# Performance work log

Hardware: AMD Instinct MI355X
Metric: run time of the kernel (lower is better)

The kernel has to match this reference:

```python
import jax, jax.numpy as jnp
import numpy as np

S = 2048       # num tokens (one sequence)
H = 2048       # hidden size
D = 64         # head dim
HQ_SWA, HQ_HSA = 24, 8
HK_SWA, HK_HSA = 6, 2
WINDOW = 512   # sliding window size
THETA = 1e6
EPS = 1e-6
SCALE = D ** -0.5
NEG = -1e9


def setup_inputs() -> dict:
    key = jax.random.key(0)
    ks = jax.random.split(key, 9)
    def w(k, fan_in, fan_out):
        return jax.random.normal(k, (fan_in, fan_out), jnp.float32) * (1.0 / np.sqrt(fan_in))
    return {
        "hidden_states": jax.random.normal(ks[0], (S, H), jnp.float32),
        "positions": jnp.arange(S, dtype=jnp.int32),
        "wq_swa": w(ks[1], H, HQ_SWA * D),
        "wk_swa": w(ks[2], H, HK_SWA * D),
        "wv_swa": w(ks[3], H, HK_SWA * D),
        "wq_hsa": w(ks[4], H, HQ_HSA * D),
        "wk_hsa": w(ks[5], H, HK_HSA * D),
        "wv_hsa": w(ks[6], H, HK_HSA * D),
        "q_norm_w": jnp.ones((D,), jnp.float32),
        "k_norm_w": jnp.ones((D,), jnp.float32),
        "wo": w(ks[7], (HQ_SWA + HQ_HSA) * D, H),
    }


def _rmsnorm(x, w):
    # per-head RMSNorm over last dim (head_dim)
    var = jnp.mean(x * x, axis=-1, keepdims=True)
    return x * jax.lax.rsqrt(var + EPS) * w


def _rope(x, positions):
    # neox-style RoPE on [S, h, D]
    half = D // 2
    inv_freq = 1.0 / (THETA ** (jnp.arange(half, dtype=jnp.float32) / half))
    ang = positions.astype(jnp.float32)[:, None] * inv_freq  # [S, half]
    cos = jnp.cos(ang)[:, None, :]
    sin = jnp.sin(ang)[:, None, :]
    x1, x2 = x[..., :half], x[..., half:]
    return jnp.concatenate([x1 * cos - x2 * sin, x2 * cos + x1 * sin], axis=-1)


def _gqa_attn(q, k, v, mask):
    # q: [S, hq, D], k/v: [S, hk, D], mask: [S, S] bool (True = attend)
    hk = k.shape[1]
    g = q.shape[1] // hk
    qh = q.reshape(S, hk, g, D)
    scores = jnp.einsum('qhgd,khd->hgqk', qh, k) * SCALE
    scores = jnp.where(mask[None, None], scores, NEG)
    p = jax.nn.softmax(scores, axis=-1)
    out = jnp.einsum('hgqk,khd->qhgd', p, v)
    return out.reshape(S, hk * g * D)


def reference(hidden_states, positions, wq_swa, wk_swa, wv_swa,
              wq_hsa, wk_hsa, wv_hsa, q_norm_w, k_norm_w, wo):
    x = hidden_states
    # projections -> per-head layout
    swa_q = (x @ wq_swa).reshape(S, HQ_SWA, D)
    swa_k = (x @ wk_swa).reshape(S, HK_SWA, D)
    swa_v = (x @ wv_swa).reshape(S, HK_SWA, D)
    hsa_q = (x @ wq_hsa).reshape(S, HQ_HSA, D)
    hsa_k = (x @ wk_hsa).reshape(S, HK_HSA, D)
    hsa_v = (x @ wv_hsa).reshape(S, HK_HSA, D)
    # per-head RMSNorm on q and k (layerwise_qk_norm = False)
    swa_q = _rmsnorm(swa_q, q_norm_w)
    swa_k = _rmsnorm(swa_k, k_norm_w)
    hsa_q = _rmsnorm(hsa_q, q_norm_w)
    hsa_k = _rmsnorm(hsa_k, k_norm_w)
    # RoPE on SWA branch only (apply_hsa_rope = False)
    swa_q = _rope(swa_q, positions)
    swa_k = _rope(swa_k, positions)
    # masks
    i = jnp.arange(S)[:, None]
    j = jnp.arange(S)[None, :]
    causal = j <= i
    swa_mask = causal & ((i - j) < WINDOW)
    # SWA branch: sliding-window causal attention
    swa_out = _gqa_attn(swa_q, swa_k, swa_v, swa_mask)   # [S, HQ_SWA*D]
    # HSA branch: full-causal GQA attention (reference: all blocks retrieved)
    hsa_out = _gqa_attn(hsa_q, hsa_k, hsa_v, causal)     # [S, HQ_HSA*D]
    attn_out = jnp.concatenate([swa_out, hsa_out], axis=-1)
    return attn_out @ wo
```

## Files before the change

kernel.cpp:

```cpp
#include <hip/hip_runtime.h>

#define S_LEN 2048
#define QKV_N 3072

typedef __bf16 bf16_t;
typedef bf16_t b16x8 __attribute__((ext_vector_type(8)));
typedef unsigned short u16x8 __attribute__((ext_vector_type(8)));
typedef float f32x4 __attribute__((ext_vector_type(4)));
typedef unsigned int u32;
typedef __attribute__((address_space(3))) u32 lds_u32;
typedef __attribute__((address_space(1))) const u32 g_u32;

__device__ __forceinline__ void gload16(void* l, const void* g){
  __builtin_amdgcn_global_load_lds((g_u32*)g, (lds_u32*)l, 16, 0, 0);
}

__device__ __forceinline__ unsigned short f2b(float f){
  u32 u = __builtin_bit_cast(u32, f);
  u += 0x7fffu + ((u >> 16) & 1u);
  return (unsigned short)(u >> 16);
}

__global__ __launch_bounds__(256) void k_cvt(const float* __restrict__ x,
                                             unsigned short* __restrict__ y){
  int i = (blockIdx.x * 256 + threadIdx.x) * 4;
  float4 v = *reinterpret_cast<const float4*>(x + i);
  ushort4 o; o.x = f2b(v.x); o.y = f2b(v.y); o.z = f2b(v.z); o.w = f2b(v.w);
  *reinterpret_cast<ushort4*>(y + i) = o;
}

__global__ __launch_bounds__(256) void k_transpose(const float* __restrict__ W,
                                                   unsigned short* __restrict__ Wt,
                                                   int Ncols, int nOff){
  __shared__ float t[64][65];
  int tx = threadIdx.x & 15, ty = threadIdx.x >> 4;
  int n0 = blockIdx.x * 64, k0 = blockIdx.y * 64;
#pragma unroll
  for (int s2 = 0; s2 < 4; ++s2){
    int kr = ty + s2*16;
    float4 v = *reinterpret_cast<const float4*>(W + (size_t)(k0+kr)*Ncols + n0 + tx*4);
    t[kr][tx*4+0]=v.x; t[kr][tx*4+1]=v.y; t[kr][tx*4+2]=v.z; t[kr][tx*4+3]=v.w;
  }
  __syncthreads();
#pragma unroll
  for (int s2 = 0; s2 < 4; ++s2){
    int nr = ty + s2*16;
    ushort4 o;
    o.x = f2b(t[tx*4+0][nr]); o.y = f2b(t[tx*4+1][nr]);
    o.z = f2b(t[tx*4+2][nr]); o.w = f2b(t[tx*4+3][nr]);
    *reinterpret_cast<ushort4*>(Wt + (size_t)(nOff + n0 + nr)*2048 + k0 + tx*4) = o;
  }
}

__global__ __launch_bounds__(256) void k_vt(const float* __restrict__ QKV,
                                            unsigned short* __restrict__ Vt){
  __shared__ float t[64][65];
  int h = blockIdx.y, s0 = blockIdx.x * 64;
  int base = (h < 6) ? (1920 + 64*h) : (2944 + 64*(h-6));
  int tx = threadIdx.x & 15, ty = threadIdx.x >> 4;
#pragma unroll
  for (int it = 0; it < 4; ++it){
    int r = ty + it*16;
    float4 v = *reinterpret_cast<const float4*>(QKV + (size_t)(s0+r)*QKV_N + base + tx*4);
    t[r][tx*4+0]=v.x; t[r][tx*4+1]=v.y; t[r][tx*4+2]=v.z; t[r][tx*4+3]=v.w;
  }
  __syncthreads();
#pragma unroll
  for (int it = 0; it < 4; ++it){
    int d = ty + it*16;
    ushort4 o;
    o.x = f2b(t[tx*4+0][d]); o.y = f2b(t[tx*4+1][d]);
    o.z = f2b(t[tx*4+2][d]); o.w = f2b(t[tx*4+3][d]);
    *reinterpret_cast<ushort4*>(Vt + ((size_t)h*64 + d)*S_LEN + s0 + tx*4) = o;
  }
}

__global__ __launch_bounds__(256) void k_gemm_bt(const unsigned short* __restrict__ A,
                                                const unsigned short* __restrict__ Bt,
                                                float* __restrict__ C,
                                                int M, int N, int K){
  __shared__ unsigned short As[128*32];
  __shared__ unsigned short Bs[128*32];
  const int tid = threadIdx.x, lane = tid & 63, w = tid >> 6;
  const int wr = w >> 1, wc = w & 1;
  const int l15 = lane & 15, lq = lane >> 4;
  const int rowA0 = blockIdx.y * 128, rowB0 = blockIdx.x * 128;
  const int scol = (lane & 3) * 8;
  f32x4 acc[4][4];
  f32x4 z4 = {0.f,0.f,0.f,0.f};
#pragma unroll
  for (int m=0;m<4;++m)
#pragma unroll
    for (int n=0;n<4;++n) acc[m][n] = z4;
  const int srow = lane >> 2;
  for (int k0 = 0; k0 < K; k0 += 32){
    __syncthreads();
#pragma unroll
    for (int i = 0; i < 2; ++i){
      int r = w*32 + i*16 + srow;
      gload16(&As[(w*32 + i*16)*32], A  + (size_t)(rowA0 + r)*K + k0 + scol);
      gload16(&Bs[(w*32 + i*16)*32], Bt + (size_t)(rowB0 + r)*K + k0 + scol);
    }
    __syncthreads();
    b16x8 af[4], bfr[4];
#pragma unroll
    for (int m=0;m<4;++m)
      af[m] = *reinterpret_cast<const b16x8*>(&As[(wr*64 + m*16 + l15)*32 + lq*8]);
#pragma unroll
    for (int n=0;n<4;++n)
      bfr[n] = *reinterpret_cast<const b16x8*>(&Bs[(wc*64 + n*16 + l15)*32 + lq*8]);
#pragma unroll
    for (int m=0;m<4;++m)
#pragma unroll
      for (int n=0;n<4;++n)
        acc[m][n] = __builtin_amdgcn_mfma_f32_16x16x32_bf16(af[m], bfr[n], acc[m][n], 0,0,0);
  }
  const int rB = rowA0 + wr*64, cB = rowB0 + wc*64;
#pragma unroll
  for (int m=0;m<4;++m)
#pragma unroll
    for (int n=0;n<4;++n)
#pragma unroll
      for (int r=0;r<4;++r)
        C[(size_t)(rB + m*16 + lq*4 + r)*N + cB + n*16 + l15] = acc[m][n][r];
}

__global__ __launch_bounds__(256) void k_normrope(const float* __restrict__ QKV,
    const int* __restrict__ pos, const float* __restrict__ qw, const float* __restrict__ kw,
    unsigned short* __restrict__ Qb, unsigned short* __restrict__ Kb){
  int job = blockIdx.x * 4 + (threadIdx.x >> 6);
  int row = blockIdx.y;
  int d = threadIdx.x & 63;
  int srcCol; unsigned short* dst; const float* wn = qw; int rope = 0, qscale = 0;
  if (job < 24){ srcCol = job*64; dst = Qb + ((size_t)job*S_LEN + row)*64; rope = 1; qscale = 1; }
  else if (job < 30){ int h=job-24; srcCol = 1536 + h*64; dst = Kb + ((size_t)h*S_LEN + row)*64; wn = kw; rope = 1; }
  else if (job < 38){ int h=job-30; srcCol = 2304 + h*64; dst = Qb + ((size_t)(24+h)*S_LEN + row)*64; qscale = 1; }
  else { int h=job-38; srcCol = 2816 + h*64; dst = Kb + ((size_t)(6+h)*S_LEN + row)*64; wn = kw; }
  float x = QKV[(size_t)row*QKV_N + srcCol + d];
  float ss = x*x;
#pragma unroll
  for (int m=1;m<64;m<<=1) ss += __shfl_xor(ss, m);
  float y = x * rsqrtf(ss*(1.0f/64.0f) + 1e-6f) * wn[d];
  if (rope){
    int i = d & 31;
    float inv = expf(-(float)i * (13.815510557964274f * (1.0f/32.0f)));
    float ang = (float)pos[row] * inv;
    float c = cosf(ang), sn = sinf(ang);
    float partner = __shfl_xor(y, 32);
    y = (d < 32) ? (y*c - partner*sn) : (y*c + partner*sn);
  }
  if (qscale) y *= 0.125f;
  dst[d] = f2b(y);
}

__global__ __launch_bounds__(256,2) void k_attn(const unsigned short* __restrict__ Qb,
    const unsigned short* __restrict__ Kb, const unsigned short* __restrict__ Vtg,
    unsigned short* __restrict__ Ob){
  __shared__ unsigned short Ks[64*64];
  __shared__ unsigned short Vs[64*64];
  __shared__ unsigned short Pw[4][32*72];
  const int tid = threadIdx.x, lane = tid & 63, w = tid >> 6;
  const int l15 = lane & 15, lq = lane >> 4;
  int bid = blockIdx.x, kvi, qt;
  if (bid < 128){ kvi = 6 + (bid & 1); qt = 63 - (bid >> 1); }
  else { int r = bid - 128; kvi = r % 6; qt = r / 6; }
  const bool swa = (kvi < 6);
  const int qh = swa ? (kvi*4 + w) : (24 + (kvi-6)*4 + w);
  const int q0 = qt * 32;
  const unsigned short* Qh = Qb + (size_t)qh*S_LEN*64;
  const unsigned short* Kh = Kb + (size_t)kvi*S_LEN*64;
  const unsigned short* Vh = Vtg + (size_t)kvi*64*S_LEN;
  b16x8 qf[2][2];
#pragma unroll
  for (int qm=0;qm<2;++qm)
#pragma unroll
    for (int h=0;h<2;++h)
      qf[qm][h] = *reinterpret_cast<const b16x8*>(Qh + (size_t)(q0+qm*16+l15)*64 + h*32 + lq*8);
  f32x4 z4 = {0.f,0.f,0.f,0.f};
  f32x4 o[4][2];
#pragma unroll
  for (int dm=0;dm<4;++dm){ o[dm][0]=z4; o[dm][1]=z4; }
  float mrun[2] = {-1e30f,-1e30f};
  float lrun[2] = {0.f,0.f};
  int jstart = 0;
  if (swa){ jstart = q0 - 511; if (jstart < 0) jstart = 0; jstart &= ~63; }
  const int jend = q0 + 32;
  for (int j0 = jstart; j0 < jend; j0 += 64){
    __syncthreads();
#pragma unroll
    for (int it = 0; it < 2; ++it){
      int slot = tid + it*256;
      int r = (slot >> 3), g = (slot & 7) ^ (r & 7);
      gload16(&Ks[(size_t)(it*256 + w*64)*8], Kh + (size_t)(j0 + r)*64 + g*8);
      gload16(&Vs[(size_t)(it*256 + w*64)*8], Vh + (size_t)r*S_LEN + j0 + g*8);
    }
    __syncthreads();
    b16x8 kf[4][2];
#pragma unroll
    for (int ct=0;ct<4;++ct)
#pragma unroll
      for (int h=0;h<2;++h)
        kf[ct][h] = *reinterpret_cast<const b16x8*>(
          &Ks[(ct*16 + l15)*64 + (((h*4 + lq) ^ (l15 & 7)) << 3)]);
    f32x4 s[2][4];
#pragma unroll
    for (int qm=0;qm<2;++qm)
#pragma unroll
      for (int ct=0;ct<4;++ct){
        f32x4 acc = z4;
        acc = __builtin_amdgcn_mfma_f32_16x16x32_bf16(kf[ct][0], qf[qm][0], acc, 0,0,0);
        acc = __builtin_amdgcn_mfma_f32_16x16x32_bf16(kf[ct][1], qf[qm][1], acc, 0,0,0);
        s[qm][ct] = acc;
      }
#pragma unroll
    for (int qm=0;qm<2;++qm){
      const int q = q0 + qm*16 + l15;
      const bool full = (j0 + 63 <= q0 + qm*16) &&
                        (!swa || (j0 >= q0 + qm*16 + 15 - 511));
      if (!full){
#pragma unroll
        for (int ct=0;ct<4;++ct)
#pragma unroll
          for (int r=0;r<4;++r){
            int kv = j0 + ct*16 + lq*4 + r;
            bool v = (kv <= q) && (!swa || (q - kv < 512));
            if (!v) s[qm][ct][r] = -1e30f;
          }
      }
      float pmax = s[qm][0][0];
#pragma unroll
      for (int ct=0;ct<4;++ct)
#pragma unroll
        for (int r=0;r<4;++r) pmax = fmaxf(pmax, s[qm][ct][r]);
      pmax = fmaxf(pmax, __shfl_xor(pmax, 16));
      pmax = fmaxf(pmax, __shfl_xor(pmax, 32));
      float mnew = fmaxf(mrun[qm], pmax);
      float f = __expf(mrun[qm] - mnew);
      mrun[qm] = mnew;
      float psum = 0.f;
#pragma unroll
      for (int ct=0;ct<4;++ct){
#pragma unroll
        for (int r=0;r<4;++r){
          float sv = s[qm][ct][r];
          float p = (sv > -0.5e30f) ? __expf(sv - mnew) : 0.f;
          s[qm][ct][r] = p;
          psum += p;
        }
#pragma unroll
        for (int u=0;u<2;++u){
          u32 dw = ((u32)f2b(s[qm][ct][2*u])) | (((u32)f2b(s[qm][ct][2*u+1])) << 16);
          *reinterpret_cast<u32*>(&Pw[w][(qm*16 + l15)*72 + ct*16 + lq*4 + 2*u]) = dw;
        }
      }
      psum += __shfl_xor(psum, 16);
      psum += __shfl_xor(psum, 32);
      lrun[qm] = lrun[qm]*f + psum;
#pragma unroll
      for (int dm=0;dm<4;++dm)
#pragma unroll
        for (int r=0;r<4;++r) o[dm][qm][r] *= f;
    }
    b16x8 vf[4][2];
#pragma unroll
    for (int dm=0;dm<4;++dm)
#pragma unroll
      for (int ks=0;ks<2;++ks)
        vf[dm][ks] = *reinterpret_cast<const b16x8*>(
          &Vs[(dm*16 + l15)*64 + (((ks*4 + lq) ^ (l15 & 7)) << 3)]);
    b16x8 pb[2][2];
#pragma unroll
    for (int qm=0;qm<2;++qm)
#pragma unroll
      for (int ks=0;ks<2;++ks)
        pb[qm][ks] = *reinterpret_cast<const b16x8*>(&Pw[w][(qm*16 + l15)*72 + ks*32 + lq*8]);
#pragma unroll
    for (int dm=0;dm<4;++dm)
#pragma unroll
      for (int qm=0;qm<2;++qm){
        o[dm][qm] = __builtin_amdgcn_mfma_f32_16x16x32_bf16(vf[dm][0], pb[qm][0], o[dm][qm], 0,0,0);
        o[dm][qm] = __builtin_amdgcn_mfma_f32_16x16x32_bf16(vf[dm][1], pb[qm][1], o[dm][qm], 0,0,0);
      }
  }
#pragma unroll
  for (int qm=0;qm<2;++qm){
    float inv = 1.0f / lrun[qm];
    const size_t rowb = (size_t)(q0 + qm*16 + l15) * 2048 + qh*64;
#pragma unroll
    for (int dm=0;dm<4;++dm){
      ushort4 ov;
      ov.x = f2b(o[dm][qm][0]*inv); ov.y = f2b(o[dm][qm][1]*inv);
      ov.z = f2b(o[dm][qm][2]*inv); ov.w = f2b(o[dm][qm][3]*inv);
      *reinterpret_cast<ushort4*>(Ob + rowb + dm*16 + lq*4) = ov;
    }
  }
}

extern "C" void kernel_launch(void* const* d_in, const int* in_sizes, int n_in,
                              void* d_out, int out_size, void* d_ws, size_t ws_size,
                              hipStream_t stream){
  const float* x      = (const float*)d_in[0];
  const int*   pos    = (const int*)d_in[1];
  const float* wq_swa = (const float*)d_in[2];
  const float* wk_swa = (const float*)d_in[3];
  const float* wv_swa = (const float*)d_in[4];
  const float* wq_hsa = (const float*)d_in[5];
  const float* wk_hsa = (const float*)d_in[6];
  const float* wv_hsa = (const float*)d_in[7];
  const float* qw     = (const float*)d_in[8];
  const float* kw     = (const float*)d_in[9];
  const float* wo     = (const float*)d_in[10];
  char* ws = (char*)d_ws;
  unsigned short* xb  = (unsigned short*)(ws);
  unsigned short* Wt  = (unsigned short*)(ws + 8388608);
  unsigned short* WoT = (unsigned short*)(ws + 20971520);
  float*          QKV = (float*)(ws + 29360128);
  unsigned short* Qb  = (unsigned short*)(ws + 54525952);
  unsigned short* Kb  = (unsigned short*)(ws + 62914560);
  unsigned short* Vtg = (unsigned short*)(ws + 65011712);
  unsigned short* Ab  = (unsigned short*)(ws + 67108864);
  float* out = (float*)d_out;

  k_cvt<<<4096, 256, 0, stream>>>(x, xb);
  k_transpose<<<dim3(24,32), 256, 0, stream>>>(wq_swa, Wt, 1536, 0);
  k_transpose<<<dim3(6,32),  256, 0, stream>>>(wk_swa, Wt, 384, 1536);
  k_transpose<<<dim3(6,32),  256, 0, stream>>>(wv_swa, Wt, 384, 1920);
  k_transpose<<<dim3(8,32),  256, 0, stream>>>(wq_hsa, Wt, 512, 2304);
  k_transpose<<<dim3(2,32),  256, 0, stream>>>(wk_hsa, Wt, 128, 2816);
  k_transpose<<<dim3(2,32),  256, 0, stream>>>(wv_hsa, Wt, 128, 2944);
  k_transpose<<<dim3(32,32), 256, 0, stream>>>(wo, WoT, 2048, 0);
  k_gemm_bt<<<dim3(24,16), 256, 0, stream>>>(xb, Wt, QKV, 2048, 3072, 2048);
  k_normrope<<<dim3(10,2048), 256, 0, stream>>>(QKV, pos, qw, kw, Qb, Kb);
  k_vt<<<dim3(32,8), 256, 0, stream>>>(QKV, Vtg);
  k_attn<<<512, 256, 0, stream>>>(Qb, Kb, Vtg, Ab);
  k_gemm_bt<<<dim3(16,16), 256, 0, stream>>>(Ab, WoT, out, 2048, 2048, 2048);
}
```

Measured before the change: 308.7 us.

## Double-buffer GEMM and attention tiles, shrink KV tile, fuse QKV weight transposes

After: 300.9 us. -2.5%, faster.

```diff
diff --git a/kernel.cpp b/kernel.cpp
--- a/kernel.cpp
+++ b/kernel.cpp
@@ -5,7 +5,6 @@
 
 typedef __bf16 bf16_t;
 typedef bf16_t b16x8 __attribute__((ext_vector_type(8)));
-typedef unsigned short u16x8 __attribute__((ext_vector_type(8)));
 typedef float f32x4 __attribute__((ext_vector_type(4)));
 typedef unsigned int u32;
 typedef __attribute__((address_space(3))) u32 lds_u32;
@@ -52,6 +51,39 @@
   }
 }
 
+__global__ __launch_bounds__(256) void k_transpose_qkv(
+    const float* __restrict__ wq_s, const float* __restrict__ wk_s,
+    const float* __restrict__ wv_s, const float* __restrict__ wq_h,
+    const float* __restrict__ wk_h, const float* __restrict__ wv_h,
+    unsigned short* __restrict__ Wt){
+  __shared__ float t[64][65];
+  int n0 = blockIdx.x * 64, k0 = blockIdx.y * 64;
+  const float* W; int Ncols, base;
+  if      (n0 < 1536){ W = wq_s; Ncols = 1536; base = 0;    }
+  else if (n0 < 1920){ W = wk_s; Ncols = 384;  base = 1536; }
+  else if (n0 < 2304){ W = wv_s; Ncols = 384;  base = 1920; }
+  else if (n0 < 2816){ W = wq_h; Ncols = 512;  base = 2304; }
+  else if (n0 < 2944){ W = wk_h; Ncols = 128;  base = 2816; }
+  else               { W = wv_h; Ncols = 128;  base = 2944; }
+  int nl = n0 - base;
+  int tx = threadIdx.x & 15, ty = threadIdx.x >> 4;
+#pragma unroll
+  for (int s2 = 0; s2 < 4; ++s2){
+    int kr = ty + s2*16;
+    float4 v = *reinterpret_cast<const float4*>(W + (size_t)(k0+kr)*Ncols + nl + tx*4);
+    t[kr][tx*4+0]=v.x; t[kr][tx*4+1]=v.y; t[kr][tx*4+2]=v.z; t[kr][tx*4+3]=v.w;
+  }
+  __syncthreads();
+#pragma unroll
+  for (int s2 = 0; s2 < 4; ++s2){
+    int nr = ty + s2*16;
+    ushort4 o;
+    o.x = f2b(t[tx*4+0][nr]); o.y = f2b(t[tx*4+1][nr]);
+    o.z = f2b(t[tx*4+2][nr]); o.w = f2b(t[tx*4+3][nr]);
+    *reinterpret_cast<ushort4*>(Wt + (size_t)(n0 + nr)*2048 + k0 + tx*4) = o;
+  }
+}
+
 __global__ __launch_bounds__(256) void k_vt(const float* __restrict__ QKV,
                                             unsigned short* __restrict__ Vt){
   __shared__ float t[64][65];
@@ -79,41 +111,50 @@
                                                 const unsigned short* __restrict__ Bt,
                                                 float* __restrict__ C,
                                                 int M, int N, int K){
-  __shared__ unsigned short As[128*32];
-  __shared__ unsigned short Bs[128*32];
+  __shared__ unsigned short As[2][128*32];
+  __shared__ unsigned short Bs[2][128*32];
   const int tid = threadIdx.x, lane = tid & 63, w = tid >> 6;
   const int wr = w >> 1, wc = w & 1;
   const int l15 = lane & 15, lq = lane >> 4;
   const int rowA0 = blockIdx.y * 128, rowB0 = blockIdx.x * 128;
-  const int scol = (lane & 3) * 8;
+  const int srow = lane >> 2, scol = (lane & 3) * 8;
   f32x4 acc[4][4];
   f32x4 z4 = {0.f,0.f,0.f,0.f};
 #pragma unroll
   for (int m=0;m<4;++m)
 #pragma unroll
     for (int n=0;n<4;++n) acc[m][n] = z4;
-  const int srow = lane >> 2;
+#pragma unroll
+  for (int i = 0; i < 2; ++i){
+    int r = w*32 + i*16 + srow;
+    gload16(&As[0][(w*32 + i*16)*32], A  + (size_t)(rowA0 + r)*K + scol);
+    gload16(&Bs[0][(w*32 + i*16)*32], Bt + (size_t)(rowB0 + r)*K + scol);
+  }
+  __syncthreads();
+  int cur = 0;
   for (int k0 = 0; k0 < K; k0 += 32){
-    __syncthreads();
-#pragma unroll
-    for (int i = 0; i < 2; ++i){
-      int r = w*32 + i*16 + srow;
-      gload16(&As[(w*32 + i*16)*32], A  + (size_t)(rowA0 + r)*K + k0 + scol);
-      gload16(&Bs[(w*32 + i*16)*32], Bt + (size_t)(rowB0 + r)*K + k0 + scol);
+    if (k0 + 32 < K){
+#pragma unroll
+      for (int i = 0; i < 2; ++i){
+        int r = w*32 + i*16 + srow;
+        gload16(&As[cur^1][(w*32 + i*16)*32], A  + (size_t)(rowA0 + r)*K + k0 + 32 + scol);
+        gload16(&Bs[cur^1][(w*32 + i*16)*32], Bt + (size_t)(rowB0 + r)*K + k0 + 32 + scol);
+      }
     }
-    __syncthreads();
     b16x8 af[4], bfr[4];
 #pragma unroll
     for (int m=0;m<4;++m)
-      af[m] = *reinterpret_cast<const b16x8*>(&As[(wr*64 + m*16 + l15)*32 + lq*8]);
+      af[m] = *reinterpret_cast<const b16x8*>(&As[cur][(wr*64 + m*16 + l15)*32 + lq*8]);
 #pragma unroll
     for (int n=0;n<4;++n)
-      bfr[n] = *reinterpret_cast<const b16x8*>(&Bs[(wc*64 + n*16 + l15)*32 + lq*8]);
+      bfr[n] = *reinterpret_cast<const b16x8*>(&Bs[cur][(wc*64 + n*16 + l15)*32 + lq*8]);
 #pragma unroll
     for (int m=0;m<4;++m)
 #pragma unroll
       for (int n=0;n<4;++n)
         acc[m][n] = __builtin_amdgcn_mfma_f32_16x16x32_bf16(af[m], bfr[n], acc[m][n], 0,0,0);
+    __syncthreads();
+    cur ^= 1;
   }
   const int rB = rowA0 + wr*64, cB = rowB0 + wc*64;
 #pragma unroll
@@ -153,12 +194,12 @@
   dst[d] = f2b(y);
 }
 
-__global__ __launch_bounds__(256,2) void k_attn(const unsigned short* __restrict__ Qb,
+__global__ __launch_bounds__(256,3) void k_attn(const unsigned short* __restrict__ Qb,
     const unsigned short* __restrict__ Kb, const unsigned short* __restrict__ Vtg,
     unsigned short* __restrict__ Ob){
-  __shared__ unsigned short Ks[64*64];
-  __shared__ unsigned short Vs[64*64];
-  __shared__ unsigned short Pw[4][32*72];
+  __shared__ unsigned short Ks[2][32*64];
+  __shared__ unsigned short Vs[2][64*32];
+  __shared__ unsigned short Pw[4][32*40];
   const int tid = threadIdx.x, lane = tid & 63, w = tid >> 6;
   const int l15 = lane & 15, lq = lane >> 4;
   int bid = blockIdx.x, kvi, qt;
@@ -183,30 +224,32 @@
   float mrun[2] = {-1e30f,-1e30f};
   float lrun[2] = {0.f,0.f};
   int jstart = 0;
-  if (swa){ jstart = q0 - 511; if (jstart < 0) jstart = 0; jstart &= ~63; }
+  if (swa){ jstart = q0 - 511; if (jstart < 0) jstart = 0; jstart &= ~31; }
   const int jend = q0 + 32;
-  for (int j0 = jstart; j0 < jend; j0 += 64){
-    __syncthreads();
-#pragma unroll
-    for (int it = 0; it < 2; ++it){
-      int slot = tid + it*256;
-      int r = (slot >> 3), g = (slot & 7) ^ (r & 7);
-      gload16(&Ks[(size_t)(it*256 + w*64)*8], Kh + (size_t)(j0 + r)*64 + g*8);
-      gload16(&Vs[(size_t)(it*256 + w*64)*8], Vh + (size_t)r*S_LEN + j0 + g*8);
+  const int rK = tid >> 3, gK = ((tid & 7) ^ (rK & 7)) * 8;
+  const int dV = tid >> 2, gV = ((tid & 3) ^ (dV & 3)) * 8;
+  const int ldsW = w * 512;
+  gload16(&Ks[0][ldsW], Kh + (size_t)(jstart + rK)*64 + gK);
+  gload16(&Vs[0][ldsW], Vh + (size_t)dV*S_LEN + jstart + gV);
+  __syncthreads();
+  int cur = 0;
+  for (int j0 = jstart; j0 < jend; j0 += 32){
+    if (j0 + 32 < jend){
+      gload16(&Ks[cur^1][ldsW], Kh + (size_t)(j0 + 32 + rK)*64 + gK);
+      gload16(&Vs[cur^1][ldsW], Vh + (size_t)dV*S_LEN + j0 + 32 + gV);
     }
-    __syncthreads();
-    b16x8 kf[4][2];
-#pragma unroll
-    for (int ct=0;ct<4;++ct)
+    b16x8 kf[2][2];
+#pragma unroll
+    for (int ct=0;ct<2;++ct)
 #pragma unroll
       for (int h=0;h<2;++h)
         kf[ct][h] = *reinterpret_cast<const b16x8*>(
-          &Ks[(ct*16 + l15)*64 + (((h*4 + lq) ^ (l15 & 7)) << 3)]);
-    f32x4 s[2][4];
+          &Ks[cur][(ct*16 + l15)*64 + (((h*4 + lq) ^ (l15 & 7)) << 3)]);
+    f32x4 s[2][2];
 #pragma unroll
     for (int qm=0;qm<2;++qm)
 #pragma unroll
-      for (int ct=0;ct<4;++ct){
+      for (int ct=0;ct<2;++ct){
         f32x4 acc = z4;
         acc = __builtin_amdgcn_mfma_f32_16x16x32_bf16(kf[ct][0], qf[qm][0], acc, 0,0,0);
         acc = __builtin_amdgcn_mfma_f32_16x16x32_bf16(kf[ct][1], qf[qm][1], acc, 0,0,0);
@@ -215,11 +258,11 @@
 #pragma unroll
     for (int qm=0;qm<2;++qm){
       const int q = q0 + qm*16 + l15;
-      const bool full = (j0 + 63 <= q0 + qm*16) &&
+      const bool full = (j0 + 31 <= q0 + qm*16) &&
                         (!swa || (j0 >= q0 + qm*16 + 15 - 511));
       if (!full){
 #pragma unroll
-        for (int ct=0;ct<4;++ct)
+        for (int ct=0;ct<2;++ct)
 #pragma unroll
           for (int r=0;r<4;++r){
             int kv = j0 + ct*16 + lq*4 + r;
@@ -229,7 +272,7 @@
       }
       float pmax = s[qm][0][0];
 #pragma unroll
-      for (int ct=0;ct<4;++ct)
+      for (int ct=0;ct<2;++ct)
 #pragma unroll
         for (int r=0;r<4;++r) pmax = fmaxf(pmax, s[qm][ct][r]);
       pmax = fmaxf(pmax, __shfl_xor(pmax, 16));
@@ -239,7 +282,7 @@
       mrun[qm] = mnew;
       float psum = 0.f;
 #pragma unroll
-      for (int ct=0;ct<4;++ct){
+      for (int ct=0;ct<2;++ct){
 #pragma unroll
         for (int r=0;r<4;++r){
           float sv = s[qm][ct][r];
@@ -250,7 +293,7 @@
 #pragma unroll
         for (int u=0;u<2;++u){
           u32 dw = ((u32)f2b(s[qm][ct][2*u])) | (((u32)f2b(s[qm][ct][2*u+1])) << 16);
-          *reinterpret_cast<u32*>(&Pw[w][(qm*16 + l15)*72 + ct*16 + lq*4 + 2*u]) = dw;
+          *reinterpret_cast<u32*>(&Pw[w][(qm*16 + l15)*40 + ct*16 + lq*4 + 2*u]) = dw;
         }
       }
       psum += __shfl_xor(psum, 16);
@@ -261,26 +304,22 @@
 #pragma unroll
         for (int r=0;r<4;++r) o[dm][qm][r] *= f;
     }
-    b16x8 vf[4][2];
+    b16x8 vf[4];
 #pragma unroll
     for (int dm=0;dm<4;++dm)
-#pragma unroll
-      for (int ks=0;ks<2;++ks)
-        vf[dm][ks] = *reinterpret_cast<const b16x8*>(
-          &Vs[(dm*16 + l15)*64 + (((ks*4 + lq) ^ (l15 & 7)) << 3)]);
-    b16x8 pb[2][2];
+      vf[dm] = *reinterpret_cast<const b16x8*>(
+        &Vs[cur][(dm*16 + l15)*32 + ((lq ^ (l15 & 3)) << 3)]);
+    b16x8 pb[2];
 #pragma unroll
     for (int qm=0;qm<2;++qm)
-#pragma unroll
-      for (int ks=0;ks<2;++ks)
-        pb[qm][ks] = *reinterpret_cast<const b16x8*>(&Pw[w][(qm*16 + l15)*72 + ks*32 + lq*8]);
+      pb[qm] = *reinterpret_cast<const b16x8*>(&Pw[w][(qm*16 + l15)*40 + lq*8]);
 #pragma unroll
     for (int dm=0;dm<4;++dm)
 #pragma unroll
-      for (int qm=0;qm<2;++qm){
-        o[dm][qm] = __builtin_amdgcn_mfma_f32_16x16x32_bf16(vf[dm][0], pb[qm][0], o[dm][qm], 0,0,0);
-        o[dm][qm] = __builtin_amdgcn_mfma_f32_16x16x32_bf16(vf[dm][1], pb[qm][1], o[dm][qm], 0,0,0);
-      }
+      for (int qm=0;qm<2;++qm)
+        o[dm][qm] = __builtin_amdgcn_mfma_f32_16x16x32_bf16(vf[dm], pb[qm], o[dm][qm], 0,0,0);
+    __syncthreads();
+    cur ^= 1;
   }
 #pragma unroll
   for (int qm=0;qm<2;++qm){
@@ -322,12 +361,8 @@
   float* out = (float*)d_out;
 
   k_cvt<<<4096, 256, 0, stream>>>(x, xb);
-  k_transpose<<<dim3(24,32), 256, 0, stream>>>(wq_swa, Wt, 1536, 0);
-  k_transpose<<<dim3(6,32),  256, 0, stream>>>(wk_swa, Wt, 384, 1536);
-  k_transpose<<<dim3(6,32),  256, 0, stream>>>(wv_swa, Wt, 384, 1920);
-  k_transpose<<<dim3(8,32),  256, 0, stream>>>(wq_hsa, Wt, 512, 2304);
-  k_transpose<<<dim3(2,32),  256, 0, stream>>>(wk_hsa, Wt, 128, 2816);
-  k_transpose<<<dim3(2,32),  256, 0, stream>>>(wv_hsa, Wt, 128, 2944);
+  k_transpose_qkv<<<dim3(48,32), 256, 0, stream>>>(wq_swa, wk_swa, wv_swa,
+                                                   wq_hsa, wk_hsa, wv_hsa, Wt);
   k_transpose<<<dim3(32,32), 256, 0, stream>>>(wo, WoT, 2048, 0);
   k_gemm_bt<<<dim3(24,16), 256, 0, stream>>>(xb, Wt, QKV, 2048, 3072, 2048);
   k_normrope<<<dim3(10,2048), 256, 0, stream>>>(QKV, pos, qw, kw, Qb, Kb);
```
